# Kernel tuning notes

Hardware: AMD Instinct MI355X
Metric: run time of the kernel (lower is better)

## Reference

```python
import jax, jax.numpy as jnp
import numpy as np
from functools import partial

NUM_CLASSES = 4
HEAD_OUTS = [4, 2, 1, 3, 2, 2]  # class, offset, z, size, yaw, vel -> sum 14
VOXEL = (0.1, 0.1)
PC_RANGE = (0.0, -39.68, -3.0, 100.0, 39.68, 1.0)
MIN_RADIUS = 2.0
BN_EPS = 1e-5


def setup_inputs() -> dict:
    key = jax.random.key(0)
    ks = jax.random.split(key, 12)
    B, C, H, W, N = 4, 256, 200, 200, 128
    spatial_features = jax.random.normal(ks[0], (B, C, H, W), jnp.float32)
    # gt boxes: x,y,z,w,l,h,yaw,cls,vx,vy ; coords chosen so grid idx in [0,200)
    x = jax.random.uniform(ks[1], (B, N), jnp.float32, 0.5, 19.5)
    y = jax.random.uniform(ks[2], (B, N), jnp.float32, -39.0, -20.0)
    z = jax.random.uniform(ks[3], (B, N), jnp.float32, -2.0, 0.0)
    dims = jax.random.uniform(ks[4], (B, N, 3), jnp.float32, 1.0, 4.0)
    yaw = jax.random.uniform(ks[5], (B, N), jnp.float32, -3.14159, 3.14159)
    cls = jax.random.randint(ks[6], (B, N), 0, NUM_CLASSES).astype(jnp.float32)
    vel = 0.1 * jax.random.normal(ks[7], (B, N, 2), jnp.float32)
    gt = jnp.concatenate([x[..., None], y[..., None], z[..., None], dims,
                          yaw[..., None], cls[..., None], vel], axis=-1)
    # zero out last 16 boxes per sample -> filtered by validity mask
    gt = gt.at[:, -16:, :].set(0.0)
    w1 = 0.05 * jax.random.normal(ks[8], (6, C, C, 3, 3), jnp.float32)
    bn_gamma = jnp.ones((6, C), jnp.float32)
    bn_beta = jnp.zeros((6, C), jnp.float32)
    bn_mean = 0.1 * jax.random.normal(ks[9], (6, C), jnp.float32)
    bn_var = jax.random.uniform(ks[10], (6, C), jnp.float32, 0.5, 1.5)
    w2 = 0.05 * jax.random.normal(ks[11], (14, C, 1, 1), jnp.float32)
    b2 = jnp.zeros((14,), jnp.float32)
    return {"spatial_features": spatial_features, "gt_boxes": gt, "w1": w1,
            "bn_gamma": bn_gamma, "bn_beta": bn_beta, "bn_mean": bn_mean,
            "bn_var": bn_var, "w2": w2, "b2": b2}


def _conv(x, w, pad):
    return jax.lax.conv_general_dilated(x, w, (1, 1), pad,
                                        dimension_numbers=("NCHW", "OIHW", "NCHW"))


def _heads(x, w1, g, b, m, v, w2, b2):
    outs, o = [], 0
    for i, nout in enumerate(HEAD_OUTS):
        h = _conv(x, w1[i], "SAME")  # [B,C,H,W]
        h = g[i][None, :, None, None] * (h - m[i][None, :, None, None]) \
            * jax.lax.rsqrt(v[i][None, :, None, None] + BN_EPS) + b[i][None, :, None, None]
        h = jax.nn.relu(h)
        outs.append(_conv(h, w2[o:o + nout], "VALID") + b2[o:o + nout][None, :, None, None])
        o += nout
    return jnp.concatenate(outs, axis=1)  # [B,14,H,W]


def _targets(gt, H, W):
    B, N = gt.shape[:2]
    x, y, z = gt[..., 0], gt[..., 1], gt[..., 2]
    bw, bl, bh = gt[..., 3], gt[..., 4], gt[..., 5]
    yaw = gt[..., 6]
    cls = jnp.clip(gt[..., 7].astype(jnp.int32), 0, NUM_CLASSES - 1)
    vel = gt[..., 8:10]
    valid = (jnp.abs(x) + jnp.abs(y) + jnp.abs(z)) > 0
    gx = (x - PC_RANGE[0]) / VOXEL[0]
    gy = (y - PC_RANGE[1]) / VOXEL[1]
    gxi = jnp.floor(gx).astype(jnp.int32)
    gyi = jnp.floor(gy).astype(jnp.int32)
    valid = valid & (gxi >= 0) & (gxi < W) & (gyi >= 0) & (gyi < H)
    xoff = gx - gxi.astype(gx.dtype)
    yoff = gy - gyi.astype(gy.dtype)
    # scalar targets scatter (invalid boxes dropped via out-of-range flat index)
    vals = jnp.stack([xoff, yoff, z, bw, bl, bh, jnp.sin(yaw), jnp.cos(yaw),
                      vel[..., 0], vel[..., 1], jnp.ones_like(x)], axis=-1)  # [B,N,11]
    bidx = jnp.broadcast_to(jnp.arange(B, dtype=jnp.int32)[:, None], (B, N))
    flat = bidx * (H * W) + gyi * W + gxi
    flat = jnp.where(valid, flat, B * H * W)  # out of range -> dropped
    scat = jnp.zeros((B * H * W, 11), jnp.float32)
    scat = scat.at[flat.reshape(-1)].set(vals.reshape(-1, 11), mode="drop")
    scalars = scat.reshape(B, H, W, 11).transpose(0, 3, 1, 2)  # [B,11,H,W]
    # gaussian heatmap: per-box splat, scatter-max into class channel
    sigma = jnp.maximum(jnp.sqrt(bw ** 2 + bl ** 2) / 2.0, MIN_RADIUS) / 3.0  # [B,N]
    xs = jnp.arange(W, dtype=jnp.float32)
    ys = jnp.arange(H, dtype=jnp.float32)
    d2 = (xs[None, None, None, :] - gxi[..., None, None].astype(jnp.float32)) ** 2 + \
         (ys[None, None, :, None] - gyi[..., None, None].astype(jnp.float32)) ** 2  # [B,N,H,W]
    gauss = jnp.exp(-d2 / (2.0 * sigma[..., None, None] ** 2))
    gauss = jnp.where(valid[..., None, None], gauss, 0.0)
    heat = jnp.zeros((B, NUM_CLASSES, H, W), jnp.float32)
    heat = heat.at[bidx, cls].max(gauss)
    return jnp.concatenate([heat, scalars], axis=1)  # [B,15,H,W]


def reference(spatial_features, gt_boxes, w1, bn_gamma, bn_beta, bn_mean, bn_var, w2, b2):
    H, W = spatial_features.shape[-2:]
    preds = _heads(spatial_features, w1, bn_gamma, bn_beta, bn_mean, bn_var, w2, b2)
    tgts = _targets(gt_boxes, H, W)
    return jnp.concatenate([preds, tgts], axis=1)  # [B,29,H,W]
```

## Files before the change

kernel.cpp:

```cpp
#include <hip/hip_runtime.h>

typedef __attribute__((ext_vector_type(8))) short short8;
typedef __attribute__((ext_vector_type(4))) float f32x4;
typedef __attribute__((ext_vector_type(4))) unsigned short us4;
typedef __attribute__((ext_vector_type(8))) unsigned short us8;

union FragU { short8 s; us4 h[2]; us8 u; };

__device__ __forceinline__ unsigned short f2bf(float f) {
  union { float f; unsigned int u; } v; v.f = f;
  unsigned int r = (v.u + 0x7fffu + ((v.u >> 16) & 1u)) >> 16;
  return (unsigned short)r;
}

typedef const __attribute__((address_space(1))) unsigned int* gas1_t;
typedef __attribute__((address_space(3))) unsigned int* las3_t;
__device__ __forceinline__ void glds16(const void* g, void* l) {
  __builtin_amdgcn_global_load_lds((gas1_t)g, (las3_t)l, 16, 0, 0);
}

__global__ void transpose_pad_k(const float* __restrict__ sf, unsigned short* __restrict__ Xtp) {
  __shared__ float tile[32][33];
  int b = blockIdx.z, c0 = blockIdx.y * 32, p0 = blockIdx.x * 32;
  int tx = threadIdx.x, ty = threadIdx.y;
#pragma unroll
  for (int i = 0; i < 4; ++i)
    tile[ty + i * 8][tx] = sf[((size_t)(b * 256 + c0 + ty + i * 8) * 40000) + p0 + tx];
  __syncthreads();
#pragma unroll
  for (int i = 0; i < 4; ++i) {
    int p = p0 + ty + i * 8;
    int y = p / 200, x = p - y * 200;
    size_t pf = (size_t)b * 40804 + (size_t)(y + 1) * 202 + (x + 1);
    Xtp[(pf << 8) + c0 + tx] = f2bf(tile[tx][ty + i * 8]);
  }
}

__global__ void prep_w1f_k(const float* __restrict__ w1, const float* __restrict__ gamma,
                           const float* __restrict__ var, unsigned short* __restrict__ W1f) {
  int id = blockIdx.x * 256 + threadIdx.x;
  if (id >= 6 * 256 * 2304) return;
  int k = id % 2304;
  int rest = id / 2304;
  int oc = rest & 255, h = rest >> 8;
  int tap = k >> 8, c = k & 255;
  int hc = h * 256 + oc;
  float s = gamma[hc] * rsqrtf(var[hc] + 1e-5f);
  W1f[id] = f2bf(s * w1[(hc * 256 + c) * 9 + tap]);
}

__global__ __launch_bounds__(256, 2) void conv_head_v4_k(
    const unsigned short* __restrict__ Xtp, const unsigned short* __restrict__ W1f,
    const float* __restrict__ gamma, const float* __restrict__ beta,
    const float* __restrict__ mean, const float* __restrict__ var,
    const float* __restrict__ w2, const float* __restrict__ b2,
    float* __restrict__ out) {
  const int NOUT[6] = {4, 2, 1, 3, 2, 2};
  const int OFFS[6] = {0, 4, 6, 7, 10, 12};
  __shared__ __align__(16) char smem[76032];
  unsigned short* h_s  = (unsigned short*)smem;
  unsigned short* w2_s = (unsigned short*)(smem + 67584);

  int tid = threadIdx.x;
  int head = blockIdx.z, b = blockIdx.y;
  int p_loc = blockIdx.x * 128;
  int nout = NOUT[head], ooff = OFFS[head];

  int wid = tid >> 6, lane = tid & 63;
  int wm = wid >> 1, wn = wid & 1;
  int l15 = lane & 15, lhi = lane >> 4;

  {
    int j = tid >> 4, cb = (tid & 15) * 16;
    us8 t0, t1;
#pragma unroll
    for (int q = 0; q < 8; ++q) {
      t0[q] = (j < nout) ? f2bf(w2[(ooff + j) * 256 + cb + q]) : (unsigned short)0;
      t1[q] = (j < nout) ? f2bf(w2[(ooff + j) * 256 + cb + 8 + q]) : (unsigned short)0;
    }
    *(us8*)&w2_s[j * 264 + cb] = t0;
    *(us8*)&w2_s[j * 264 + cb + 8] = t1;
  }

  int r0 = tid >> 2;
  int cbsw = (((tid & 3) ^ ((tid >> 3) & 3)) << 4);
  int pA0 = p_loc + r0;       if (pA0 > 39999) pA0 = 39999;
  int pA1 = p_loc + r0 + 64;  if (pA1 > 39999) pA1 = 39999;
  int ay0 = pA0 / 200, ax0 = pA0 - ay0 * 200;
  int ay1 = pA1 / 200, ax1 = pA1 - ay1 * 200;
  const char* xb = (const char*)Xtp + (size_t)b * 40804 * 512;
  const char* As0 = xb + (size_t)((ay0 + 1) * 202 + ax0 + 1) * 512 + cbsw;
  const char* As1 = xb + (size_t)((ay1 + 1) * 202 + ax1 + 1) * 512 + cbsw;

  const char* Bs0 = (const char*)W1f + (size_t)(head * 256 + r0) * 4608 + cbsw;
  const char* Bs1 = Bs0 + (size_t)64 * 4608;
  const char* Bs2 = Bs0 + (size_t)128 * 4608;
  const char* Bs3 = Bs0 + (size_t)192 * 4608;

  char* ALd[2] = {smem + wid * 1024, smem + 24576 + wid * 1024};
  char* BLd[2] = {smem + 8192 + wid * 1024, smem + 32768 + wid * 1024};

  f32x4 acc[4][8];
#pragma unroll
  for (int mi = 0; mi < 4; ++mi)
#pragma unroll
    for (int ni = 0; ni < 8; ++ni) acc[mi][ni] = (f32x4){0.f, 0.f, 0.f, 0.f};

  {
    long ab = -203L * 512;
    glds16(As0 + ab, ALd[0]);
    glds16(As1 + ab, ALd[0] + 4096);
    glds16(Bs0, BLd[0]);
    glds16(Bs1, BLd[0] + 4096);
    glds16(Bs2, BLd[0] + 8192);
    glds16(Bs3, BLd[0] + 12288);
  }
  __syncthreads();

  int slotA = (lhi ^ ((l15 >> 1) & 3)) * 8;

  for (int kt = 0; kt < 72; ++kt) {
    int cur = kt & 1;
    if (kt < 71) {
      int kn = kt + 1;
      int tap = kn >> 3;
      int c0b = (kn & 7) << 6;
      int t3 = tap / 3;
      int doff = (t3 - 1) * 202 + (tap - t3 * 3 - 1);
      long ab = (long)doff * 512 + c0b;
      long bb = (long)kn * 64;
      glds16(As0 + ab, ALd[cur ^ 1]);
      glds16(As1 + ab, ALd[cur ^ 1] + 4096);
      glds16(Bs0 + bb, BLd[cur ^ 1]);
      glds16(Bs1 + bb, BLd[cur ^ 1] + 4096);
      glds16(Bs2 + bb, BLd[cur ^ 1] + 8192);
      glds16(Bs3 + bb, BLd[cur ^ 1] + 12288);
    }
    const unsigned short* A_sh = (const unsigned short*)(smem + (cur ? 24576 : 0));
    const unsigned short* B_sh = (const unsigned short*)(smem + (cur ? 32768 : 8192));
    short8 af[4], bfr[8];
#pragma unroll
    for (int mi = 0; mi < 4; ++mi) {
      FragU u;
      u.u = *(const us8*)&A_sh[(wm * 64 + mi * 16 + l15) * 32 + slotA];
      af[mi] = u.s;
    }
#pragma unroll
    for (int ni = 0; ni < 8; ++ni) {
      FragU u;
      u.u = *(const us8*)&B_sh[(wn * 128 + ni * 16 + l15) * 32 + slotA];
      bfr[ni] = u.s;
    }
#pragma unroll
    for (int mi = 0; mi < 4; ++mi)
#pragma unroll
      for (int ni = 0; ni < 8; ++ni)
        acc[mi][ni] = __builtin_amdgcn_mfma_f32_16x16x32_bf16(af[mi], bfr[ni], acc[mi][ni], 0, 0, 0);
    __syncthreads();
  }

  {
    float tbr[8];
#pragma unroll
    for (int ni = 0; ni < 8; ++ni) {
      int hc = head * 256 + wn * 128 + ni * 16 + l15;
      float s = gamma[hc] * rsqrtf(var[hc] + 1e-5f);
      tbr[ni] = beta[hc] - s * mean[hc];
    }
#pragma unroll
    for (int mi = 0; mi < 4; ++mi)
#pragma unroll
      for (int ni = 0; ni < 8; ++ni)
#pragma unroll
        for (int r = 0; r < 4; ++r)
          acc[mi][ni][r] = fmaxf(acc[mi][ni][r] + tbr[ni], 0.f);
  }
#pragma unroll
  for (int mi = 0; mi < 4; ++mi) {
#pragma unroll
    for (int ni = 0; ni < 8; ++ni) {
      int ocl = wn * 128 + ni * 16 + l15;
#pragma unroll
      for (int r = 0; r < 4; ++r) {
        int px = wm * 64 + mi * 16 + lhi * 4 + r;
        h_s[px * 264 + ocl] = f2bf(acc[mi][ni][r]);
      }
    }
  }
  __syncthreads();

#pragma unroll
  for (int g2 = 0; g2 < 2; ++g2) {
    int grp = wid * 2 + g2;
    float b2v = (l15 < nout) ? b2[ooff + l15] : 0.f;
    f32x4 oacc = (f32x4){0.f, 0.f, 0.f, 0.f};
#pragma unroll
    for (int kc = 0; kc < 8; ++kc) {
      int koff = kc * 32 + lhi * 8;
      FragU hu, wu;
      hu.u = *(const us8*)&h_s[(grp * 16 + l15) * 264 + koff];
      wu.u = *(const us8*)&w2_s[l15 * 264 + koff];
      oacc = __builtin_amdgcn_mfma_f32_16x16x32_bf16(hu.s, wu.s, oacc, 0, 0, 0);
    }
    if (l15 < nout) {
      float* dst = out + (size_t)(b * 29 + ooff + l15) * 40000;
#pragma unroll
      for (int r = 0; r < 4; ++r) {
        int px_g = p_loc + grp * 16 + lhi * 4 + r;
        if (px_g < 40000) dst[px_g] = oacc[r] + b2v;
      }
    }
  }
}

__global__ __launch_bounds__(512) void conv_head_nows_k(
    const float* __restrict__ sf, const float* __restrict__ w1,
    const float* __restrict__ gamma, const float* __restrict__ beta,
    const float* __restrict__ mean, const float* __restrict__ var,
    const float* __restrict__ w2, const float* __restrict__ b2,
    float* __restrict__ out) {
  const int NOUT[6] = {4, 2, 1, 3, 2, 2};
  const int OFFS[6] = {0, 4, 6, 7, 10, 12};
  __shared__ __align__(16) char smem[78080];
  unsigned short* A_s  = (unsigned short*)smem;
  unsigned short* B_s  = (unsigned short*)(smem + 9216);
  unsigned short* h_s  = (unsigned short*)smem;
  unsigned short* w2_s = (unsigned short*)(smem + 67584);
  float* tb_s          = (float*)(smem + 76032);
  float* s_s           = (float*)(smem + 77056);

  int tid = threadIdx.x;
  int head = blockIdx.z, b = blockIdx.y;
  int p_loc = blockIdx.x * 128;
  int nout = NOUT[head], ooff = OFFS[head];
  {
    int j = tid >> 5, c8 = (tid & 31) * 8;
    us8 t;
#pragma unroll
    for (int q = 0; q < 8; ++q)
      t[q] = (j < nout) ? f2bf(w2[(ooff + j) * 256 + c8 + q]) : (unsigned short)0;
    *(us8*)&w2_s[j * 264 + c8] = t;
  }
  if (tid < 256) {
    int hc = head * 256 + tid;
    float s = gamma[hc] * rsqrtf(var[hc] + 1e-5f);
    s_s[tid] = s;
    tb_s[tid] = beta[hc] - s * mean[hc];
  }
  __syncthreads();

  int wid = tid >> 6, lane = tid & 63;
  int wm = wid >> 2, wn = wid & 3;
  int l15 = lane & 15, lhi = lane >> 4;
  int cg = wid, mm = lane;
  int p0 = p_loc + mm, p1 = p0 + 64;
  int ay0 = p0 / 200, ax0 = p0 - ay0 * 200;
  int ay1 = p1 / 200, ax1 = p1 - ay1 * 200;
  const float* sfb = sf + (size_t)b * 256 * 40000;
  int oc = tid >> 1, half = tid & 1;
  const float* w1h = w1 + ((size_t)head * 256 + oc) * 2304;
  float sv = s_s[oc];

  f32x4 acc[4][4];
#pragma unroll
  for (int mi = 0; mi < 4; ++mi)
#pragma unroll
    for (int ni = 0; ni < 4; ++ni) acc[mi][ni] = (f32x4){0.f, 0.f, 0.f, 0.f};

  for (int kt = 0; kt < 72; ++kt) {
    int tap = kt >> 3;
    int c0 = (kt & 7) << 5;
    int t3 = tap / 3;
    int dy = t3 - 1, dx = tap - t3 * 3 - 1;
    {
      const float* src = sfb + (size_t)(c0 + cg * 4) * 40000;
      int yy = ay0 + dy, xx = ax0 + dx;
      us4 v = (us4){0, 0, 0, 0};
      if ((unsigned)yy < 200u && (unsigned)xx < 200u) {
        int pix = yy * 200 + xx;
        v[0] = f2bf(src[pix]);
        v[1] = f2bf(src[40000 + pix]);
        v[2] = f2bf(src[80000 + pix]);
        v[3] = f2bf(src[120000 + pix]);
      }
      *(us4*)&A_s[mm * 36 + cg * 4] = v;
      yy = ay1 + dy; xx = ax1 + dx;
      us4 w = (us4){0, 0, 0, 0};
      if ((unsigned)yy < 200u && (unsigned)xx < 200u) {
        int pix = yy * 200 + xx;
        w[0] = f2bf(src[pix]);
        w[1] = f2bf(src[40000 + pix]);
        w[2] = f2bf(src[80000 + pix]);
        w[3] = f2bf(src[120000 + pix]);
      }
      *(us4*)&A_s[(mm + 64) * 36 + cg * 4] = w;
    }
    {
      int kk = half * 16;
#pragma unroll
      for (int g = 0; g < 4; ++g) {
        us4 t;
#pragma unroll
        for (int q = 0; q < 4; ++q)
          t[q] = f2bf(sv * w1h[(c0 + kk + g * 4 + q) * 9 + tap]);
        *(us4*)&B_s[oc * 36 + kk + g * 4] = t;
      }
    }
    __syncthreads();
    short8 af[4], bfr[4];
#pragma unroll
    for (int mi = 0; mi < 4; ++mi) {
      int a = (wm * 64 + mi * 16 + l15) * 36 + lhi * 8;
      FragU u;
      u.h[0] = *(const us4*)&A_s[a];
      u.h[1] = *(const us4*)&A_s[a + 4];
      af[mi] = u.s;
    }
#pragma unroll
    for (int ni = 0; ni < 4; ++ni) {
      int a = (wn * 64 + ni * 16 + l15) * 36 + lhi * 8;
      FragU u;
      u.h[0] = *(const us4*)&B_s[a];
      u.h[1] = *(const us4*)&B_s[a + 4];
      bfr[ni] = u.s;
    }
#pragma unroll
    for (int mi = 0; mi < 4; ++mi)
#pragma unroll
      for (int ni = 0; ni < 4; ++ni)
        acc[mi][ni] = __builtin_amdgcn_mfma_f32_16x16x32_bf16(af[mi], bfr[ni], acc[mi][ni], 0, 0, 0);
    __syncthreads();
  }
#pragma unroll
  for (int mi = 0; mi < 4; ++mi) {
#pragma unroll
    for (int ni = 0; ni < 4; ++ni) {
      int ocl = wn * 64 + ni * 16 + l15;
      float tbv = tb_s[ocl];
#pragma unroll
      for (int r = 0; r < 4; ++r) {
        int px = wm * 64 + mi * 16 + lhi * 4 + r;
        float v = fmaxf(acc[mi][ni][r] + tbv, 0.f);
        h_s[px * 264 + ocl] = f2bf(v);
      }
    }
  }
  __syncthreads();
  {
    int j = l15;
    float b2v = (j < nout) ? b2[ooff + j] : 0.f;
    f32x4 oacc = (f32x4){0.f, 0.f, 0.f, 0.f};
#pragma unroll
    for (int kc = 0; kc < 8; ++kc) {
      int koff = kc * 32 + lhi * 8;
      FragU hu, wu;
      hu.u = *(const us8*)&h_s[(wid * 16 + l15) * 264 + koff];
      wu.u = *(const us8*)&w2_s[l15 * 264 + koff];
      oacc = __builtin_amdgcn_mfma_f32_16x16x32_bf16(hu.s, wu.s, oacc, 0, 0, 0);
    }
    if (j < nout) {
      float* dst = out + (size_t)(b * 29 + ooff + j) * 40000;
#pragma unroll
      for (int r = 0; r < 4; ++r) {
        int px_g = p_loc + wid * 16 + lhi * 4 + r;
        if (px_g < 40000) dst[px_g] = oacc[r] + b2v;
      }
    }
  }
}

__global__ void heat_k(const float* __restrict__ gt, float* __restrict__ out) {
  __shared__ float bx[128], by[128], binv[128];
  __shared__ int bcls[128];
  int b = blockIdx.y, tid = threadIdx.x;
  if (tid < 128) {
    const float* g = gt + (b * 128 + tid) * 10;
    float x = g[0], y = g[1], z = g[2];
    bool valid = fabsf(x) + fabsf(y) + fabsf(z) > 0.f;
    float gx = x / 0.1f;
    float gy = (y + 39.68f) / 0.1f;
    float fx = floorf(gx), fy = floorf(gy);
    int gxi = (int)fx, gyi = (int)fy;
    valid = valid && gxi >= 0 && gxi < 200 && gyi >= 0 && gyi < 200;
    float bw = g[3], bl = g[4];
    float sigma = fmaxf(sqrtf(bw * bw + bl * bl) * 0.5f, 2.0f) / 3.0f;
    binv[tid] = valid ? 1.f / (2.f * sigma * sigma) : -1.f;
    bx[tid] = fx;
    by[tid] = fy;
    bcls[tid] = min(max((int)g[7], 0), 3);
  }
  __syncthreads();
  int pid = blockIdx.x * 256 + tid;
  if (pid >= 40000) return;
  float py = (float)(pid / 200);
  float px = (float)(pid - (pid / 200) * 200);
  float h0 = 0.f, h1 = 0.f, h2 = 0.f, h3 = 0.f;
  for (int n = 0; n < 128; ++n) {
    float inv = binv[n];
    if (inv < 0.f) continue;
    float ddx = px - bx[n], ddy = py - by[n];
    float t = (ddx * ddx + ddy * ddy) * inv;
    if (t > 40.f) continue;
    float e = __expf(-t);
    int c = bcls[n];
    h0 = fmaxf(h0, c == 0 ? e : 0.f);
    h1 = fmaxf(h1, c == 1 ? e : 0.f);
    h2 = fmaxf(h2, c == 2 ? e : 0.f);
    h3 = fmaxf(h3, c == 3 ? e : 0.f);
  }
  int base = (b * 29 + 14) * 40000 + pid;
  out[base] = h0;
  out[base + 40000] = h1;
  out[base + 80000] = h2;
  out[base + 120000] = h3;
#pragma unroll
  for (int q = 0; q < 11; ++q) out[base + (4 + q) * 40000] = 0.f;
}

__global__ void scatter_k(const float* __restrict__ gt, float* __restrict__ out) {
  int b = threadIdx.x;
  if (b >= 4) return;
  for (int n = 0; n < 128; ++n) {
    const float* g = gt + (b * 128 + n) * 10;
    float x = g[0], y = g[1], z = g[2];
    if (!(fabsf(x) + fabsf(y) + fabsf(z) > 0.f)) continue;
    float gx = x / 0.1f;
    float gy = (y + 39.68f) / 0.1f;
    float fx = floorf(gx), fy = floorf(gy);
    int gxi = (int)fx, gyi = (int)fy;
    if (gxi < 0 || gxi >= 200 || gyi < 0 || gyi >= 200) continue;
    int base = (b * 29 + 18) * 40000 + gyi * 200 + gxi;
    out[base] = gx - fx;
    out[base + 1 * 40000] = gy - fy;
    out[base + 2 * 40000] = z;
    out[base + 3 * 40000] = g[3];
    out[base + 4 * 40000] = g[4];
    out[base + 5 * 40000] = g[5];
    out[base + 6 * 40000] = sinf(g[6]);
    out[base + 7 * 40000] = cosf(g[6]);
    out[base + 8 * 40000] = g[8];
    out[base + 9 * 40000] = g[9];
    out[base + 10 * 40000] = 1.f;
  }
}

extern "C" void kernel_launch(void* const* d_in, const int* in_sizes, int n_in,
                              void* d_out, int out_size, void* d_ws, size_t ws_size,
                              hipStream_t stream) {
  const float* sf    = (const float*)d_in[0];
  const float* gt    = (const float*)d_in[1];
  const float* w1    = (const float*)d_in[2];
  const float* gamma = (const float*)d_in[3];
  const float* beta  = (const float*)d_in[4];
  const float* mean  = (const float*)d_in[5];
  const float* var   = (const float*)d_in[6];
  const float* w2    = (const float*)d_in[7];
  const float* b2    = (const float*)d_in[8];
  float* out = (float*)d_out;
  char* ws = (char*)d_ws;

  const size_t W1F_BYTES = (size_t)6 * 256 * 2304 * 2;
  const size_t XTP_BYTES = (size_t)4 * 40804 * 256 * 2;
  unsigned short* W1f = (unsigned short*)ws;

  dim3 cgrid(313, 4, 6);
  if (ws_size >= W1F_BYTES + XTP_BYTES) {
    unsigned short* Xtp = (unsigned short*)(ws + W1F_BYTES);
    prep_w1f_k<<<(6 * 256 * 2304 + 255) / 256, 256, 0, stream>>>(w1, gamma, var, W1f);
    hipMemsetAsync(Xtp, 0, XTP_BYTES, stream);
    transpose_pad_k<<<dim3(1250, 8, 4), dim3(32, 8), 0, stream>>>(sf, Xtp);
    conv_head_v4_k<<<cgrid, 256, 0, stream>>>(Xtp, W1f, gamma, beta, mean, var, w2, b2, out);
  } else {
    conv_head_nows_k<<<cgrid, 512, 0, stream>>>(sf, w1, gamma, beta, mean, var, w2, b2, out);
  }
  heat_k<<<dim3(157, 4), 256, 0, stream>>>(gt, out);
  scatter_k<<<1, 64, 0, stream>>>(gt, out);
}
```

Before: 1.284 ms.

## Triple-buffer conv GEMM loads with explicit vmcnt waits and MFMA priority

The implicit-GEMM conv main loop moves from double buffering to a three-stage LDS ring, prefetching two k-tiles ahead. Each stage is gated by a counted s_waitcnt vmcnt and raw s_barrier, which replaces the full __syncthreads drain. MFMAs run under raised s_setprio, and the w2 fragments for the 1x1 head now sit in registers instead of LDS. The goal is to hide global-to-LDS latency behind more in-flight loads. In exchange it uses more LDS and more registers, and correctness relies on the hand-counted vmcnt values matching the six loads issued per stage.

Measured after the change: 1.224 ms. 4.7% less time.

```diff
diff --git a/kernel.cpp b/kernel.cpp
--- a/kernel.cpp
+++ b/kernel.cpp
@@ -49,7 +49,7 @@
   W1f[id] = f2bf(s * w1[(hc * 256 + c) * 9 + tap]);
 }
 
-__global__ __launch_bounds__(256, 2) void conv_head_v4_k(
+__global__ __launch_bounds__(256, 2) void conv_head_v5_k(
     const unsigned short* __restrict__ Xtp, const unsigned short* __restrict__ W1f,
     const float* __restrict__ gamma, const float* __restrict__ beta,
     const float* __restrict__ mean, const float* __restrict__ var,
@@ -57,9 +57,8 @@
     float* __restrict__ out) {
   const int NOUT[6] = {4, 2, 1, 3, 2, 2};
   const int OFFS[6] = {0, 4, 6, 7, 10, 12};
-  __shared__ __align__(16) char smem[76032];
-  unsigned short* h_s  = (unsigned short*)smem;
-  unsigned short* w2_s = (unsigned short*)(smem + 67584);
+  __shared__ __align__(16) char smem[73728];
+  unsigned short* h_s = (unsigned short*)smem;
 
   int tid = threadIdx.x;
   int head = blockIdx.z, b = blockIdx.y;
@@ -69,18 +68,6 @@
   int wid = tid >> 6, lane = tid & 63;
   int wm = wid >> 1, wn = wid & 1;
   int l15 = lane & 15, lhi = lane >> 4;
-
-  {
-    int j = tid >> 4, cb = (tid & 15) * 16;
-    us8 t0, t1;
-#pragma unroll
-    for (int q = 0; q < 8; ++q) {
-      t0[q] = (j < nout) ? f2bf(w2[(ooff + j) * 256 + cb + q]) : (unsigned short)0;
-      t1[q] = (j < nout) ? f2bf(w2[(ooff + j) * 256 + cb + 8 + q]) : (unsigned short)0;
-    }
-    *(us8*)&w2_s[j * 264 + cb] = t0;
-    *(us8*)&w2_s[j * 264 + cb + 8] = t1;
-  }
 
   int r0 = tid >> 2;
   int cbsw = (((tid & 3) ^ ((tid >> 3) & 3)) << 4);
@@ -97,8 +84,24 @@
   const char* Bs2 = Bs0 + (size_t)128 * 4608;
   const char* Bs3 = Bs0 + (size_t)192 * 4608;
 
-  char* ALd[2] = {smem + wid * 1024, smem + 24576 + wid * 1024};
-  char* BLd[2] = {smem + 8192 + wid * 1024, smem + 32768 + wid * 1024};
+  char* rA = smem;
+  char* rB = smem + 24576;
+  char* rC = smem + 49152;
+
+  auto STAGE = [&](int kn, char* dst) {
+    int tap = kn >> 3;
+    int c0b = (kn & 7) << 6;
+    int t3 = tap / 3;
+    int doff = (t3 - 1) * 202 + (tap - t3 * 3 - 1);
+    long ab = (long)doff * 512 + c0b;
+    long bb = (long)kn * 64;
+    glds16(As0 + ab, dst + wid * 1024);
+    glds16(As1 + ab, dst + wid * 1024 + 4096);
+    glds16(Bs0 + bb, dst + 8192 + wid * 1024);
+    glds16(Bs1 + bb, dst + 8192 + wid * 1024 + 4096);
+    glds16(Bs2 + bb, dst + 8192 + wid * 1024 + 8192);
+    glds16(Bs3 + bb, dst + 8192 + wid * 1024 + 12288);
+  };
 
   f32x4 acc[4][8];
 #pragma unroll
@@ -106,38 +109,22 @@
 #pragma unroll
     for (int ni = 0; ni < 8; ++ni) acc[mi][ni] = (f32x4){0.f, 0.f, 0.f, 0.f};
 
-  {
-    long ab = -203L * 512;
-    glds16(As0 + ab, ALd[0]);
-    glds16(As1 + ab, ALd[0] + 4096);
-    glds16(Bs0, BLd[0]);
-    glds16(Bs1, BLd[0] + 4096);
-    glds16(Bs2, BLd[0] + 8192);
-    glds16(Bs3, BLd[0] + 12288);
-  }
-  __syncthreads();
+  STAGE(0, rA);
+  STAGE(1, rB);
 
   int slotA = (lhi ^ ((l15 >> 1) & 3)) * 8;
 
   for (int kt = 0; kt < 72; ++kt) {
-    int cur = kt & 1;
-    if (kt < 71) {
-      int kn = kt + 1;
-      int tap = kn >> 3;
-      int c0b = (kn & 7) << 6;
-      int t3 = tap / 3;
-      int doff = (t3 - 1) * 202 + (tap - t3 * 3 - 1);
-      long ab = (long)doff * 512 + c0b;
-      long bb = (long)kn * 64;
-      glds16(As0 + ab, ALd[cur ^ 1]);
-      glds16(As1 + ab, ALd[cur ^ 1] + 4096);
-      glds16(Bs0 + bb, BLd[cur ^ 1]);
-      glds16(Bs1 + bb, BLd[cur ^ 1] + 4096);
-      glds16(Bs2 + bb, BLd[cur ^ 1] + 8192);
-      glds16(Bs3 + bb, BLd[cur ^ 1] + 12288);
-    }
-    const unsigned short* A_sh = (const unsigned short*)(smem + (cur ? 24576 : 0));
-    const unsigned short* B_sh = (const unsigned short*)(smem + (cur ? 32768 : 8192));
+    if (kt < 70) STAGE(kt + 2, rC);
+    if (kt < 70)       asm volatile("s_waitcnt vmcnt(12)" ::: "memory");
+    else if (kt == 70) asm volatile("s_waitcnt vmcnt(6)" ::: "memory");
+    else               asm volatile("s_waitcnt vmcnt(0)" ::: "memory");
+    __builtin_amdgcn_sched_barrier(0);
+    __builtin_amdgcn_s_barrier();
+    __builtin_amdgcn_sched_barrier(0);
+
+    const unsigned short* A_sh = (const unsigned short*)rA;
+    const unsigned short* B_sh = (const unsigned short*)(rA + 8192);
     short8 af[4], bfr[8];
 #pragma unroll
     for (int mi = 0; mi < 4; ++mi) {
@@ -151,12 +138,18 @@
       u.u = *(const us8*)&B_sh[(wn * 128 + ni * 16 + l15) * 32 + slotA];
       bfr[ni] = u.s;
     }
+    __builtin_amdgcn_s_setprio(1);
 #pragma unroll
     for (int mi = 0; mi < 4; ++mi)
 #pragma unroll
       for (int ni = 0; ni < 8; ++ni)
         acc[mi][ni] = __builtin_amdgcn_mfma_f32_16x16x32_bf16(af[mi], bfr[ni], acc[mi][ni], 0, 0, 0);
-    __syncthreads();
+    __builtin_amdgcn_s_setprio(0);
+    __builtin_amdgcn_sched_barrier(0);
+    __builtin_amdgcn_s_barrier();
+    __builtin_amdgcn_sched_barrier(0);
+
+    char* t = rA; rA = rB; rB = rC; rC = t;
   }
 
   {
@@ -175,6 +168,19 @@
         for (int r = 0; r < 4; ++r)
           acc[mi][ni][r] = fmaxf(acc[mi][ni][r] + tbr[ni], 0.f);
   }
+  short8 wfr[8];
+  {
+    int jr = (l15 < nout) ? (ooff + l15) : 0;
+    const float* wrow = w2 + jr * 256;
+#pragma unroll
+    for (int kc = 0; kc < 8; ++kc) {
+      int koff = kc * 32 + lhi * 8;
+      FragU u;
+#pragma unroll
+      for (int q = 0; q < 8; ++q) u.u[q] = f2bf(wrow[koff + q]);
+      wfr[kc] = u.s;
+    }
+  }
 #pragma unroll
   for (int mi = 0; mi < 4; ++mi) {
 #pragma unroll
@@ -197,10 +203,9 @@
 #pragma unroll
     for (int kc = 0; kc < 8; ++kc) {
       int koff = kc * 32 + lhi * 8;
-      FragU hu, wu;
+      FragU hu;
       hu.u = *(const us8*)&h_s[(grp * 16 + l15) * 264 + koff];
-      wu.u = *(const us8*)&w2_s[l15 * 264 + koff];
-      oacc = __builtin_amdgcn_mfma_f32_16x16x32_bf16(hu.s, wu.s, oacc, 0, 0, 0);
+      oacc = __builtin_amdgcn_mfma_f32_16x16x32_bf16(hu.s, wfr[kc], oacc, 0, 0, 0);
     }
     if (l15 < nout) {
       float* dst = out + (size_t)(b * 29 + ooff + l15) * 40000;
@@ -469,7 +474,7 @@
     prep_w1f_k<<<(6 * 256 * 2304 + 255) / 256, 256, 0, stream>>>(w1, gamma, var, W1f);
     hipMemsetAsync(Xtp, 0, XTP_BYTES, stream);
     transpose_pad_k<<<dim3(1250, 8, 4), dim3(32, 8), 0, stream>>>(sf, Xtp);
-    conv_head_v4_k<<<cgrid, 256, 0, stream>>>(Xtp, W1f, gamma, beta, mean, var, w2, b2, out);
+    conv_head_v5_k<<<cgrid, 256, 0, stream>>>(Xtp, W1f, gamma, beta, mean, var, w2, b2, out);
   } else {
     conv_head_nows_k<<<cgrid, 512, 0, stream>>>(sf, w1, gamma, beta, mean, var, w2, b2, out);
   }
```
